# Kernel optimization log

Hardware: AMD Instinct MI355X
Metric: run time of the kernel (lower is better)

Reference implementation:

```python
import jax, jax.numpy as jnp
import numpy as np
from jax.scipy.special import gammainc

HUBREG_ITERS = 2
LAYERS = 3


def huber_psi(x, c):
    # Huber influence function: identity inside [-c, c], clipped outside.
    return jnp.where(jnp.abs(x) <= c, x, c * jnp.sign(x))


def chi2_cdf(x, df):
    return gammainc(df / 2.0, x / 2.0)


def hubreg_batched(beta, D, Y, mask, c, lamda, mu, sigma0):
    """Batched Huber regression with IRLS-style scale update.

    beta: [q, r]  one coefficient vector per regression (columns of Y)
    D:    [p, r]  shared design rows; regression j uses rows where mask[:, j] == 1
    Y:    [p, q]  targets, zero where unobserved
    mask: [p, q]  observation indicator (float)
    """
    p, r = D.shape
    cd = jax.lax.stop_gradient(c)  # original detaches c for alpha
    alpha = 0.5 * cd**2 * (1.0 - chi2_cdf(cd**2, 1.0)) + 0.5 * chi2_cdf(cd**2, 3.0)
    P = (D[:, :, None] * D[:, None, :]).reshape(p, r * r)  # [p, r^2]
    G = (mask.T @ P).reshape(-1, r, r)                     # [q, r, r]
    Ginv = jnp.linalg.inv(G)
    nobs = mask.sum(axis=0)                                # [q]
    sigma = sigma0 * jnp.ones((Y.shape[1],), Y.dtype)
    for _ in range(HUBREG_ITERS):
        R = (Y - D @ beta.T) * mask                        # masked residuals [p, q]
        psi = huber_psi(R / sigma[None, :], c)             # zero where mask is zero
        tau = jnp.sqrt((psi * psi).sum(axis=0)) / jnp.sqrt(2.0 * nobs * alpha)
        sigma = sigma * tau**lamda
        psi2 = huber_psi(R / sigma[None, :], c)
        rhs = D.T @ (psi2 * sigma[None, :])                # [r, q] = D[rows].T @ (psi*sigma)
        delta = jnp.einsum('qij,jq->qi', Ginv, rhs)
        beta = beta + mu * delta
    return beta


def setup_inputs() -> dict:
    key = jax.random.key(0)
    k1, k2, k3, k4 = jax.random.split(key, 4)
    m, n, r = 4096, 4096, 10
    U = jax.random.normal(k1, (m, r), jnp.float32)
    V = jax.random.normal(k2, (r, n), jnp.float32)
    obs = (jax.random.uniform(k3, (m, n)) < 0.5).astype(jnp.float32)
    X = jax.random.normal(k4, (m, n), jnp.float32) * obs  # zeros = missing entries
    return {
        "U": U, "V": V, "X": X,
        "c": jnp.float32(1.345), "lamda": jnp.float32(1.0),
        "mu": jnp.float32(0.5), "sigma": jnp.float32(1.0),
    }


def reference(U, V, X, c, lamda, mu, sigma):
    mask = (X != 0).astype(X.dtype)
    for _ in range(LAYERS):
        V = hubreg_batched(V.T, U, X, mask, c, lamda, mu, sigma).T
        U = hubreg_batched(U, V.T, X.T, mask.T, c, lamda, mu, sigma)
    return U @ V
```

## Files before the change

### kernel.cpp

```cpp
#include <hip/hip_runtime.h>
#include <math.h>

#define RNK 10
#define NG  55
#define TPB 256
#define TPBU 64
#define WPC 4
#define ROWS_P 64
#define ITILE 16

typedef float f2 __attribute__((ext_vector_type(2)));

__device__ __forceinline__ constexpr int tri(int a, int b) { return a*(a+1)/2 + b; }
constexpr int BASE2[10] = {0,0,1,2,4,6,9,12,16,20};

__global__ void init_kernel(const float* __restrict__ Uin, const float* __restrict__ Vin,
                            const float* __restrict__ cptr,
                            float* __restrict__ Ut, float* __restrict__ Vc,
                            float* __restrict__ Urow, float* __restrict__ Vrow,
                            float* __restrict__ Gbuf, float* __restrict__ tauacc,
                            float* __restrict__ rhs, float* __restrict__ alpha,
                            int m, int n, int qmax) {
    int idx = blockIdx.x * TPB + threadIdx.x;
    if (idx == 0) {
        float c  = *cptr;
        float A  = erff(c * 0.70710678118654752f);
        float B  = c * 0.79788456080286536f * expf(-0.5f*c*c);
        *alpha = 0.5f*c*c*(1.0f - A) + 0.5f*(A - B);
    }
    if (idx < RNK * m) { int k = idx / m, i = idx - k*m; Ut[idx] = Uin[i*RNK + k]; }
    if (idx < RNK * m) Urow[idx] = Uin[idx];
    if (idx < RNK * n) Vc[idx] = Vin[idx];
    if (idx < RNK * n) { int j = idx / RNK, k = idx - j*RNK; Vrow[idx] = Vin[k*n + j]; }
    if (idx < (NG + 1) * qmax) Gbuf[idx] = 0.0f;
    if (idx < qmax) tauacc[idx] = 0.0f;
    if (idx < RNK * qmax) rhs[idx] = 0.0f;
}

__global__ void transpose_kernel(const float* __restrict__ X, float* __restrict__ XT,
                                 int m, int n) {
    __shared__ float tile[32][33];
    int bx = blockIdx.x * 32, by = blockIdx.y * 32;
    int tx = threadIdx.x, ty = threadIdx.y;
    #pragma unroll
    for (int dy = 0; dy < 32; dy += 8)
        tile[ty+dy][tx] = X[(size_t)(by+ty+dy)*n + bx + tx];
    __syncthreads();
    #pragma unroll
    for (int dy = 0; dy < 32; dy += 8)
        XT[(size_t)(bx+ty+dy)*m + by + tx] = tile[tx][ty+dy];
}

__global__ void mask_kernel(const float* __restrict__ X, unsigned* __restrict__ maskV,
                            unsigned* __restrict__ maskU, int m, int n) {
    int wave = threadIdx.x >> 6, lane = threadIdx.x & 63;
    int jbase = blockIdx.x * 256 + wave * 64;
    int j  = jbase + lane;
    int i0 = blockIdx.y * 32;
    unsigned wv = 0;
    for (int u = 0; u < 32; ++u) {
        float x = X[(size_t)(i0+u)*n + j];
        bool nz = (x != 0.0f);
        wv |= (nz ? 1u : 0u) << u;
        unsigned long long bb = __ballot(nz);
        if (lane == 0) {
            int jw = jbase >> 5;
            maskU[(size_t)jw     * m + (i0+u)] = (unsigned)bb;
            maskU[(size_t)(jw+1) * m + (i0+u)] = (unsigned)(bb >> 32);
        }
    }
    maskV[(size_t)blockIdx.y * n + j] = wv;
}

__global__ __launch_bounds__(TPB)
void gram_kernel(const unsigned* __restrict__ mask, const float* __restrict__ Drow,
                 float* __restrict__ Gbuf, int q, int p) {
    __shared__ __align__(16) float Dld[WPC * 32][12];
    int j  = blockIdx.x * TPB + threadIdx.x;
    int w0 = blockIdx.y * WPC;
    int ib = w0 * 32;
    #pragma unroll
    for (int t = threadIdx.x; t < WPC * 32 * RNK; t += TPB) {
        int row = t / RNK, k = t - row * RNK;
        Dld[row][k] = Drow[(size_t)ib * RNK + t];
    }
    __syncthreads();
    f2 acc2[25];
    float accs[5];
    #pragma unroll
    for (int k = 0; k < 25; ++k) acc2[k] = (f2){0.0f, 0.0f};
    #pragma unroll
    for (int k = 0; k < 5; ++k) accs[k] = 0.0f;
    unsigned cnt = 0;
    unsigned wnext = mask[(size_t)w0 * q + j];
    for (int w = 0; w < WPC; ++w) {
        unsigned word = wnext;
        int wn = (w + 1 < WPC) ? (w + 1) : (WPC - 1);
        wnext = mask[(size_t)(w0 + wn) * q + j];
        cnt += __popc(word);
        #pragma unroll
        for (int u = 0; u < 32; ++u) {
            float f = (float)((word >> u) & 1u);
            f2 d2[5];
            #pragma unroll
            for (int k = 0; k < 5; ++k) d2[k] = *(const f2*)&Dld[w * 32 + u][2 * k];
            #pragma unroll
            for (int a = 0; a < RNK; ++a) {
                float da = d2[a >> 1][a & 1];
                float t  = f * da;
                f2 tv = {t, t};
                #pragma unroll
                for (int pb = 0; pb < (a + 1) / 2; ++pb)
                    acc2[BASE2[a] + pb] =
                        __builtin_elementwise_fma(tv, d2[pb], acc2[BASE2[a] + pb]);
                if ((a & 1) == 0) accs[a >> 1] = fmaf(t, da, accs[a >> 1]);
            }
        }
    }
    #pragma unroll
    for (int a = 0; a < RNK; ++a) {
        #pragma unroll
        for (int pb = 0; pb < (a + 1) / 2; ++pb) {
            atomicAdd(&Gbuf[tri(a, 2*pb)   * q + j], acc2[BASE2[a] + pb][0]);
            atomicAdd(&Gbuf[tri(a, 2*pb+1) * q + j], acc2[BASE2[a] + pb][1]);
        }
        if ((a & 1) == 0) atomicAdd(&Gbuf[tri(a, a) * q + j], accs[a >> 1]);
    }
    atomicAdd(&Gbuf[NG * q + j], (float)cnt);
}

__global__ __launch_bounds__(TPB)
void pass1_kernel(const float* __restrict__ Y, const float* __restrict__ Drow,
                  const float* __restrict__ Bm, const float* __restrict__ sigstore,
                  const float* __restrict__ sigma0p, const float* __restrict__ cptr,
                  float* __restrict__ tauacc, int q, int p, int use_store) {
    __shared__ __align__(16) float Dp[ROWS_P][12];
    int j  = blockIdx.x * TPB + threadIdx.x;
    int i0 = blockIdx.y * ROWS_P;
    for (int t = threadIdx.x; t < ROWS_P * RNK; t += TPB) {
        int row = t / RNK, k = t - row * RNK;
        Dp[row][k] = Drow[(size_t)i0 * RNK + t];
    }
    __syncthreads();
    f2 b2[5];
    #pragma unroll
    for (int k = 0; k < 5; ++k)
        b2[k] = (f2){Bm[(2*k)*q + j], Bm[(2*k+1)*q + j]};
    float csg = (*cptr) * (use_store ? sigstore[j] : *sigma0p);
    float a0 = 0.0f;
    float y[8];
    #pragma unroll
    for (int u = 0; u < 8; ++u) y[u] = Y[(size_t)(i0+u)*q + j];
    for (int g = 0; g < ROWS_P; g += 8) {
        float yn[8];
        if (g + 8 < ROWS_P) {
            #pragma unroll
            for (int u = 0; u < 8; ++u) yn[u] = Y[(size_t)(i0+g+8+u)*q + j];
        } else {
            #pragma unroll
            for (int u = 0; u < 8; ++u) yn[u] = 0.0f;
        }
        #pragma unroll
        for (int u = 0; u < 8; ++u) {
            int rl = g + u;
            f2 dot2 = {0.0f, 0.0f};
            #pragma unroll
            for (int k = 0; k < 5; ++k) {
                f2 d2 = *(const f2*)&Dp[rl][2*k];
                dot2 = __builtin_elementwise_fma(d2, b2[k], dot2);
            }
            float dot = dot2[0] + dot2[1];
            float r = (y[u] != 0.0f) ? y[u] - dot : 0.0f;
            r = fminf(fmaxf(r, -csg), csg);
            a0 = fmaf(r, r, a0);
        }
        #pragma unroll
        for (int u = 0; u < 8; ++u) y[u] = yn[u];
    }
    atomicAdd(&tauacc[j], a0);
}

__global__ __launch_bounds__(TPB)
void pass2_kernel(const float* __restrict__ Y, const float* __restrict__ Drow,
                  const float* __restrict__ Bm, const float* __restrict__ Gbuf,
                  const float* __restrict__ tauacc, float* __restrict__ sigstore,
                  const float* __restrict__ cptr, const float* __restrict__ alphap,
                  const float* __restrict__ lamdap, const float* __restrict__ sigma0p,
                  float* __restrict__ rhs, int q, int p, int mode) {
    __shared__ __align__(16) float Dp[ROWS_P][12];
    int j  = blockIdx.x * TPB + threadIdx.x;
    int i0 = blockIdx.y * ROWS_P;
    for (int t = threadIdx.x; t < ROWS_P * RNK; t += TPB) {
        int row = t / RNK, k = t - row * RNK;
        Dp[row][k] = Drow[(size_t)i0 * RNK + t];
    }
    __syncthreads();
    f2 b2[5];
    #pragma unroll
    for (int k = 0; k < 5; ++k)
        b2[k] = (f2){Bm[(2*k)*q + j], Bm[(2*k+1)*q + j]};
    float so  = mode ? sigstore[j] : *sigma0p;
    float nb  = Gbuf[NG*q + j];
    float tau = sqrtf(tauacc[j] / (2.0f * nb * (*alphap))) / so;
    float sg  = so * powf(tau, *lamdap);
    if (mode == 0 && blockIdx.y == 0) sigstore[j] = sg;
    float csg = (*cptr) * sg;

    f2 a2[5];
    #pragma unroll
    for (int k = 0; k < 5; ++k) a2[k] = (f2){0.0f, 0.0f};
    float y[8];
    #pragma unroll
    for (int u = 0; u < 8; ++u) y[u] = Y[(size_t)(i0+u)*q + j];
    for (int g = 0; g < ROWS_P; g += 8) {
        float yn[8];
        if (g + 8 < ROWS_P) {
            #pragma unroll
            for (int u = 0; u < 8; ++u) yn[u] = Y[(size_t)(i0+g+8+u)*q + j];
        } else {
            #pragma unroll
            for (int u = 0; u < 8; ++u) yn[u] = 0.0f;
        }
        #pragma unroll
        for (int u = 0; u < 8; ++u) {
            int rl = g + u;
            f2 d2[5];
            #pragma unroll
            for (int k = 0; k < 5; ++k) d2[k] = *(const f2*)&Dp[rl][2*k];
            f2 dot2 = {0.0f, 0.0f};
            #pragma unroll
            for (int k = 0; k < 5; ++k)
                dot2 = __builtin_elementwise_fma(d2[k], b2[k], dot2);
            float dot = dot2[0] + dot2[1];
            float r = (y[u] != 0.0f) ? y[u] - dot : 0.0f;
            r = fminf(fmaxf(r, -csg), csg);
            f2 rv = {r, r};
            #pragma unroll
            for (int k = 0; k < 5; ++k)
                a2[k] = __builtin_elementwise_fma(d2[k], rv, a2[k]);
        }
        #pragma unroll
        for (int u = 0; u < 8; ++u) y[u] = yn[u];
    }
    #pragma unroll
    for (int k = 0; k < 5; ++k) {
        atomicAdd(&rhs[(2*k)*q   + j], a2[k][0]);
        atomicAdd(&rhs[(2*k+1)*q + j], a2[k][1]);
    }
}

__global__ __launch_bounds__(TPBU)
void update_kernel(float* __restrict__ Gbuf, float* __restrict__ rhs,
                   float* __restrict__ Bm, float* __restrict__ Brow,
                   const float* __restrict__ mup,
                   float* __restrict__ tauacc, int q, int zero_g) {
    int j = blockIdx.x * TPBU + threadIdx.x;
    if (j >= q) return;
    float g[NG];
    #pragma unroll
    for (int k = 0; k < NG; ++k) g[k] = Gbuf[k*q + j];
    #pragma unroll
    for (int a = 0; a < RNK; ++a) {
        #pragma unroll
        for (int b = 0; b < a; ++b) {
            float s = g[tri(a,b)];
            #pragma unroll
            for (int k = 0; k < b; ++k) s -= g[tri(a,k)] * g[tri(b,k)];
            g[tri(a,b)] = s / g[tri(b,b)];
        }
        float s = g[tri(a,a)];
        #pragma unroll
        for (int k = 0; k < a; ++k) s -= g[tri(a,k)] * g[tri(a,k)];
        g[tri(a,a)] = sqrtf(s);
    }
    float x[RNK];
    #pragma unroll
    for (int k = 0; k < RNK; ++k) x[k] = rhs[k*q + j];
    #pragma unroll
    for (int a = 0; a < RNK; ++a) {
        float s = x[a];
        #pragma unroll
        for (int k = 0; k < a; ++k) s -= g[tri(a,k)] * x[k];
        x[a] = s / g[tri(a,a)];
    }
    #pragma unroll
    for (int a = RNK-1; a >= 0; --a) {
        float s = x[a];
        #pragma unroll
        for (int k = a+1; k < RNK; ++k) s -= g[tri(k,a)] * x[k];
        x[a] = s / g[tri(a,a)];
    }
    float mu = *mup;
    #pragma unroll
    for (int k = 0; k < RNK; ++k) {
        float nb = Bm[k*q + j] + mu * x[k];
        Bm[k*q + j] = nb;
        Brow[(size_t)j*RNK + k] = nb;
    }
    tauacc[j] = 0.0f;
    #pragma unroll
    for (int k = 0; k < RNK; ++k) rhs[k*q + j] = 0.0f;
    if (zero_g) {
        #pragma unroll
        for (int k = 0; k <= NG; ++k) Gbuf[k*q + j] = 0.0f;
    }
}

__global__ void gemm_kernel(const float* __restrict__ Ut, const float* __restrict__ Vc,
                            float* __restrict__ out, int m, int n) {
    int j  = blockIdx.x * TPB + threadIdx.x;
    int i0 = blockIdx.y * ITILE;
    float v[RNK];
    #pragma unroll
    for (int k = 0; k < RNK; ++k) v[k] = Vc[k*n + j];
    for (int i = i0; i < i0 + ITILE; ++i) {
        float acc = 0.0f;
        #pragma unroll
        for (int k = 0; k < RNK; ++k) acc = fmaf(Ut[k*m + i], v[k], acc);
        out[(size_t)i*n + j] = acc;
    }
}


namespace {
struct Scratch {
    float *Ut, *Vc, *Urow, *Vrow, *Gbuf, *rhs, *sigma, *tauacc, *alpha;
    unsigned *maskV, *maskU;
};

static void hubreg(const float* Y, const unsigned* mask, const float* Drow,
                   float* Bm, float* Brow, int q, int p,
                   const float* c, const float* lamda, const float* mu, const float* sigma0,
                   const Scratch& s, hipStream_t stream) {
    dim3 gg(q / TPB, p / (32 * WPC));
    dim3 gp(q / TPB, p / ROWS_P);
    dim3 gj(q / TPBU);

    gram_kernel  <<<gg, TPB, 0, stream>>>(mask, Drow, s.Gbuf, q, p);
    pass1_kernel <<<gp, TPB, 0, stream>>>(Y, Drow, Bm, s.sigma, sigma0, c, s.tauacc, q, p, 0);
    pass2_kernel <<<gp, TPB, 0, stream>>>(Y, Drow, Bm, s.Gbuf, s.tauacc, s.sigma, c,
                                          s.alpha, lamda, sigma0, s.rhs, q, p, 0);
    update_kernel<<<gj, TPBU, 0, stream>>>(s.Gbuf, s.rhs, Bm, Brow, mu, s.tauacc, q, 0);
    pass1_kernel <<<gp, TPB, 0, stream>>>(Y, Drow, Bm, s.sigma, sigma0, c, s.tauacc, q, p, 1);
    pass2_kernel <<<gp, TPB, 0, stream>>>(Y, Drow, Bm, s.Gbuf, s.tauacc, s.sigma, c,
                                          s.alpha, lamda, sigma0, s.rhs, q, p, 1);
    update_kernel<<<gj, TPBU, 0, stream>>>(s.Gbuf, s.rhs, Bm, Brow, mu, s.tauacc, q, 1);
}
}

extern "C" void kernel_launch(void* const* d_in, const int* in_sizes, int n_in,
                              void* d_out, int out_size, void* d_ws, size_t ws_size,
                              hipStream_t stream) {
    const float* Uin    = (const float*)d_in[0];
    const float* Vin    = (const float*)d_in[1];
    const float* X      = (const float*)d_in[2];
    const float* c      = (const float*)d_in[3];
    const float* lamda  = (const float*)d_in[4];
    const float* mu     = (const float*)d_in[5];
    const float* sigma0 = (const float*)d_in[6];
    float* out = (float*)d_out;

    const int m = in_sizes[0] / RNK;
    const int n = in_sizes[1] / RNK;
    const int qmax = (m > n) ? m : n;

    float* w = (float*)d_ws;
    auto align64 = [](size_t x) { return (x + 63) & ~(size_t)63; };
    size_t off = 0;
    Scratch s;
    s.Ut     = w + off; off = align64(off + (size_t)RNK * m);
    s.Vc     = w + off; off = align64(off + (size_t)RNK * n);
    s.Urow   = w + off; off = align64(off + (size_t)RNK * m);
    s.Vrow   = w + off; off = align64(off + (size_t)RNK * n);
    s.Gbuf   = w + off; off = align64(off + (size_t)(NG + 1) * qmax);
    s.rhs    = w + off; off = align64(off + (size_t)RNK * qmax);
    s.sigma  = w + off; off = align64(off + (size_t)qmax);
    s.tauacc = w + off; off = align64(off + (size_t)qmax);
    s.alpha  = w + off; off = align64(off + 64);
    s.maskV  = (unsigned*)(w + off); off = align64(off + (size_t)(m/32) * n);
    s.maskU  = (unsigned*)(w + off); off = align64(off + (size_t)(n/32) * m);
    (void)ws_size; (void)n_in; (void)out_size;

    {
        int tot = (NG + 1) * qmax;
        init_kernel<<<(tot + TPB - 1) / TPB, TPB, 0, stream>>>(
            Uin, Vin, c, s.Ut, s.Vc, s.Urow, s.Vrow, s.Gbuf, s.tauacc, s.rhs,
            s.alpha, m, n, qmax);
    }
    transpose_kernel<<<dim3(n / 32, m / 32), dim3(32, 8), 0, stream>>>(X, out, m, n);
    mask_kernel<<<dim3(n / 256, m / 32), TPB, 0, stream>>>(X, s.maskV, s.maskU, m, n);

    for (int layer = 0; layer < 3; ++layer) {
        hubreg(X,   s.maskV, s.Urow, s.Vc, s.Vrow, n, m, c, lamda, mu, sigma0, s, stream);
        hubreg(out, s.maskU, s.Vrow, s.Ut, s.Urow, m, n, c, lamda, mu, sigma0, s, stream);
    }

    gemm_kernel<<<dim3(n / TPB, m / ITILE), TPB, 0, stream>>>(s.Ut, s.Vc, out, m, n);
}
```

Measured before the change: 938.1 us.

## Split row ranges across lane quads in gram and pass2 with shuffle reduction

The gram and pass2 kernels now give each column four lanes, each covering a different slice of rows. The four partial sums are combined with xor shuffles, and one lane per quad does the atomic adds. Each block now handles 64 columns over larger row chunks, so far fewer global atomics hit Gbuf and rhs. In exchange, adjacent lanes read mask and Y with a stride of four rows, which hurts coalescing, and the shuffle reduction adds work.

```diff
diff --git a/kernel.cpp b/kernel.cpp
--- a/kernel.cpp
+++ b/kernel.cpp
@@ -5,7 +5,11 @@
 #define NG  55
 #define TPB 256
 #define TPBU 64
-#define WPC 4
+#define GJ   64
+#define GWRD 4
+#define GROWS_B (4 * GWRD * 32)
+#define P2RPT 64
+#define ROWS_P2 (4 * P2RPT)
 #define ROWS_P 64
 #define ITILE 16
 
@@ -13,6 +17,12 @@
 
 __device__ __forceinline__ constexpr int tri(int a, int b) { return a*(a+1)/2 + b; }
 constexpr int BASE2[10] = {0,0,1,2,4,6,9,12,16,20};
+
+__device__ __forceinline__ float qsum(float v) {
+    v += __shfl_xor(v, 1);
+    v += __shfl_xor(v, 2);
+    return v;
+}
 
 __global__ void init_kernel(const float* __restrict__ Uin, const float* __restrict__ Vin,
                             const float* __restrict__ cptr,
@@ -75,12 +85,12 @@
 __global__ __launch_bounds__(TPB)
 void gram_kernel(const unsigned* __restrict__ mask, const float* __restrict__ Drow,
                  float* __restrict__ Gbuf, int q, int p) {
-    __shared__ __align__(16) float Dld[WPC * 32][12];
-    int j  = blockIdx.x * TPB + threadIdx.x;
-    int w0 = blockIdx.y * WPC;
-    int ib = w0 * 32;
-    #pragma unroll
-    for (int t = threadIdx.x; t < WPC * 32 * RNK; t += TPB) {
+    __shared__ __align__(16) float Dld[GROWS_B][12];
+    int lane = threadIdx.x & 63, wave = threadIdx.x >> 6;
+    int jo = lane >> 2, sub = lane & 3;
+    int j  = blockIdx.x * GJ + wave * 16 + jo;
+    int ib = blockIdx.y * GROWS_B;
+    for (int t = threadIdx.x; t < GROWS_B * RNK; t += TPB) {
         int row = t / RNK, k = t - row * RNK;
         Dld[row][k] = Drow[(size_t)ib * RNK + t];
     }
@@ -92,18 +102,21 @@
     #pragma unroll
     for (int k = 0; k < 5; ++k) accs[k] = 0.0f;
     unsigned cnt = 0;
+    int w0 = blockIdx.y * (4 * GWRD) + sub * GWRD;
+    const float* dbase = &Dld[sub * (GWRD * 32)][0];
     unsigned wnext = mask[(size_t)w0 * q + j];
-    for (int w = 0; w < WPC; ++w) {
+    for (int wi = 0; wi < GWRD; ++wi) {
         unsigned word = wnext;
-        int wn = (w + 1 < WPC) ? (w + 1) : (WPC - 1);
+        int wn = (wi + 1 < GWRD) ? (wi + 1) : (GWRD - 1);
         wnext = mask[(size_t)(w0 + wn) * q + j];
         cnt += __popc(word);
+        const float* drow = dbase + wi * (32 * 12);
         #pragma unroll
         for (int u = 0; u < 32; ++u) {
             float f = (float)((word >> u) & 1u);
             f2 d2[5];
             #pragma unroll
-            for (int k = 0; k < 5; ++k) d2[k] = *(const f2*)&Dld[w * 32 + u][2 * k];
+            for (int k = 0; k < 5; ++k) d2[k] = *(const f2*)(drow + u * 12 + 2 * k);
             #pragma unroll
             for (int a = 0; a < RNK; ++a) {
                 float da = d2[a >> 1][a & 1];
@@ -118,15 +131,25 @@
         }
     }
     #pragma unroll
-    for (int a = 0; a < RNK; ++a) {
-        #pragma unroll
-        for (int pb = 0; pb < (a + 1) / 2; ++pb) {
-            atomicAdd(&Gbuf[tri(a, 2*pb)   * q + j], acc2[BASE2[a] + pb][0]);
-            atomicAdd(&Gbuf[tri(a, 2*pb+1) * q + j], acc2[BASE2[a] + pb][1]);
-        }
-        if ((a & 1) == 0) atomicAdd(&Gbuf[tri(a, a) * q + j], accs[a >> 1]);
-    }
-    atomicAdd(&Gbuf[NG * q + j], (float)cnt);
+    for (int k = 0; k < 25; ++k) {
+        acc2[k][0] = qsum(acc2[k][0]);
+        acc2[k][1] = qsum(acc2[k][1]);
+    }
+    #pragma unroll
+    for (int k = 0; k < 5; ++k) accs[k] = qsum(accs[k]);
+    float fc = qsum((float)cnt);
+    if (sub == 0) {
+        #pragma unroll
+        for (int a = 0; a < RNK; ++a) {
+            #pragma unroll
+            for (int pb = 0; pb < (a + 1) / 2; ++pb) {
+                atomicAdd(&Gbuf[tri(a, 2*pb)   * q + j], acc2[BASE2[a] + pb][0]);
+                atomicAdd(&Gbuf[tri(a, 2*pb+1) * q + j], acc2[BASE2[a] + pb][1]);
+            }
+            if ((a & 1) == 0) atomicAdd(&Gbuf[tri(a, a) * q + j], accs[a >> 1]);
+        }
+        atomicAdd(&Gbuf[NG * q + j], fc);
+    }
 }
 
 __global__ __launch_bounds__(TPB)
@@ -187,10 +210,12 @@
                   const float* __restrict__ cptr, const float* __restrict__ alphap,
                   const float* __restrict__ lamdap, const float* __restrict__ sigma0p,
                   float* __restrict__ rhs, int q, int p, int mode) {
-    __shared__ __align__(16) float Dp[ROWS_P][12];
-    int j  = blockIdx.x * TPB + threadIdx.x;
-    int i0 = blockIdx.y * ROWS_P;
-    for (int t = threadIdx.x; t < ROWS_P * RNK; t += TPB) {
+    __shared__ __align__(16) float Dp[ROWS_P2][12];
+    int lane = threadIdx.x & 63, wave = threadIdx.x >> 6;
+    int jo = lane >> 2, sub = lane & 3;
+    int j  = blockIdx.x * GJ + wave * 16 + jo;
+    int i0 = blockIdx.y * ROWS_P2;
+    for (int t = threadIdx.x; t < ROWS_P2 * RNK; t += TPB) {
         int row = t / RNK, k = t - row * RNK;
         Dp[row][k] = Drow[(size_t)i0 * RNK + t];
     }
@@ -203,30 +228,32 @@
     float nb  = Gbuf[NG*q + j];
     float tau = sqrtf(tauacc[j] / (2.0f * nb * (*alphap))) / so;
     float sg  = so * powf(tau, *lamdap);
-    if (mode == 0 && blockIdx.y == 0) sigstore[j] = sg;
+    if (mode == 0 && blockIdx.y == 0 && sub == 0) sigstore[j] = sg;
     float csg = (*cptr) * sg;
 
+    int ibase = i0 + sub * P2RPT;
+    const float* dbase = &Dp[sub * P2RPT][0];
     f2 a2[5];
     #pragma unroll
     for (int k = 0; k < 5; ++k) a2[k] = (f2){0.0f, 0.0f};
     float y[8];
     #pragma unroll
-    for (int u = 0; u < 8; ++u) y[u] = Y[(size_t)(i0+u)*q + j];
-    for (int g = 0; g < ROWS_P; g += 8) {
+    for (int u = 0; u < 8; ++u) y[u] = Y[(size_t)(ibase+u)*q + j];
+    for (int g = 0; g < P2RPT; g += 8) {
         float yn[8];
-        if (g + 8 < ROWS_P) {
-            #pragma unroll
-            for (int u = 0; u < 8; ++u) yn[u] = Y[(size_t)(i0+g+8+u)*q + j];
+        if (g + 8 < P2RPT) {
+            #pragma unroll
+            for (int u = 0; u < 8; ++u) yn[u] = Y[(size_t)(ibase+g+8+u)*q + j];
         } else {
             #pragma unroll
             for (int u = 0; u < 8; ++u) yn[u] = 0.0f;
         }
+        const float* drow = dbase + g * 12;
         #pragma unroll
         for (int u = 0; u < 8; ++u) {
-            int rl = g + u;
             f2 d2[5];
             #pragma unroll
-            for (int k = 0; k < 5; ++k) d2[k] = *(const f2*)&Dp[rl][2*k];
+            for (int k = 0; k < 5; ++k) d2[k] = *(const f2*)(drow + u * 12 + 2 * k);
             f2 dot2 = {0.0f, 0.0f};
             #pragma unroll
             for (int k = 0; k < 5; ++k)
@@ -244,8 +271,15 @@
     }
     #pragma unroll
     for (int k = 0; k < 5; ++k) {
-        atomicAdd(&rhs[(2*k)*q   + j], a2[k][0]);
-        atomicAdd(&rhs[(2*k+1)*q + j], a2[k][1]);
+        a2[k][0] = qsum(a2[k][0]);
+        a2[k][1] = qsum(a2[k][1]);
+    }
+    if (sub == 0) {
+        #pragma unroll
+        for (int k = 0; k < 5; ++k) {
+            atomicAdd(&rhs[(2*k)*q   + j], a2[k][0]);
+            atomicAdd(&rhs[(2*k+1)*q + j], a2[k][1]);
+        }
     }
 }
 
@@ -332,18 +366,19 @@
                    float* Bm, float* Brow, int q, int p,
                    const float* c, const float* lamda, const float* mu, const float* sigma0,
                    const Scratch& s, hipStream_t stream) {
-    dim3 gg(q / TPB, p / (32 * WPC));
+    dim3 gg(q / GJ, p / GROWS_B);
     dim3 gp(q / TPB, p / ROWS_P);
+    dim3 gp2(q / GJ, p / ROWS_P2);
     dim3 gj(q / TPBU);
 
     gram_kernel  <<<gg, TPB, 0, stream>>>(mask, Drow, s.Gbuf, q, p);
     pass1_kernel <<<gp, TPB, 0, stream>>>(Y, Drow, Bm, s.sigma, sigma0, c, s.tauacc, q, p, 0);
-    pass2_kernel <<<gp, TPB, 0, stream>>>(Y, Drow, Bm, s.Gbuf, s.tauacc, s.sigma, c,
-                                          s.alpha, lamda, sigma0, s.rhs, q, p, 0);
+    pass2_kernel <<<gp2, TPB, 0, stream>>>(Y, Drow, Bm, s.Gbuf, s.tauacc, s.sigma, c,
+                                           s.alpha, lamda, sigma0, s.rhs, q, p, 0);
     update_kernel<<<gj, TPBU, 0, stream>>>(s.Gbuf, s.rhs, Bm, Brow, mu, s.tauacc, q, 0);
     pass1_kernel <<<gp, TPB, 0, stream>>>(Y, Drow, Bm, s.sigma, sigma0, c, s.tauacc, q, p, 1);
-    pass2_kernel <<<gp, TPB, 0, stream>>>(Y, Drow, Bm, s.Gbuf, s.tauacc, s.sigma, c,
-                                          s.alpha, lamda, sigma0, s.rhs, q, p, 1);
+    pass2_kernel <<<gp2, TPB, 0, stream>>>(Y, Drow, Bm, s.Gbuf, s.tauacc, s.sigma, c,
+                                           s.alpha, lamda, sigma0, s.rhs, q, p, 1);
     update_kernel<<<gj, TPBU, 0, stream>>>(s.Gbuf, s.rhs, Bm, Brow, mu, s.tauacc, q, 1);
 }
 }
```

Result: slower. 967.3 us (+3.1%).

## Fuse mask building into transpose and split gram rows across quad lanes

Applied to the files above, without the earlier changes.

The separate mask kernel is removed, and the transpose kernel now builds both bit-packed masks from its shared-memory tile, so X is read one time fewer. The gram kernel is restructured so that four lanes share one column, each handling a different slice of rows. Their partial sums are combined with quad shuffles before one lane issues the atomics, which cuts atomic traffic per block and gives each block more rows. The cost is extra shuffle work and more shared memory, and the mask-building threads in the transpose may hit shared-memory bank conflicts when reading tile rows.

```diff
diff --git a/kernel.cpp b/kernel.cpp
--- a/kernel.cpp
+++ b/kernel.cpp
@@ -5,7 +5,10 @@
 #define NG  55
 #define TPB 256
 #define TPBU 64
-#define WPC 4
+#define GJ   64
+#define GWRD 4
+#define GROWS_B (4 * GWRD * 32)
+#define GSUBP (GWRD * 32 * 12 + 8)
 #define ROWS_P 64
 #define ITILE 16
 
@@ -13,6 +16,12 @@
 
 __device__ __forceinline__ constexpr int tri(int a, int b) { return a*(a+1)/2 + b; }
 constexpr int BASE2[10] = {0,0,1,2,4,6,9,12,16,20};
+
+__device__ __forceinline__ float qsum(float v) {
+    v += __shfl_xor(v, 1);
+    v += __shfl_xor(v, 2);
+    return v;
+}
 
 __global__ void init_kernel(const float* __restrict__ Uin, const float* __restrict__ Vin,
                             const float* __restrict__ cptr,
@@ -38,6 +47,7 @@
 }
 
 __global__ void transpose_kernel(const float* __restrict__ X, float* __restrict__ XT,
+                                 unsigned* __restrict__ maskV, unsigned* __restrict__ maskU,
                                  int m, int n) {
     __shared__ float tile[32][33];
     int bx = blockIdx.x * 32, by = blockIdx.y * 32;
@@ -49,40 +59,32 @@
     #pragma unroll
     for (int dy = 0; dy < 32; dy += 8)
         XT[(size_t)(bx+ty+dy)*m + by + tx] = tile[tx][ty+dy];
-}
-
-__global__ void mask_kernel(const float* __restrict__ X, unsigned* __restrict__ maskV,
-                            unsigned* __restrict__ maskU, int m, int n) {
-    int wave = threadIdx.x >> 6, lane = threadIdx.x & 63;
-    int jbase = blockIdx.x * 256 + wave * 64;
-    int j  = jbase + lane;
-    int i0 = blockIdx.y * 32;
-    unsigned wv = 0;
-    for (int u = 0; u < 32; ++u) {
-        float x = X[(size_t)(i0+u)*n + j];
-        bool nz = (x != 0.0f);
-        wv |= (nz ? 1u : 0u) << u;
-        unsigned long long bb = __ballot(nz);
-        if (lane == 0) {
-            int jw = jbase >> 5;
-            maskU[(size_t)jw     * m + (i0+u)] = (unsigned)bb;
-            maskU[(size_t)(jw+1) * m + (i0+u)] = (unsigned)(bb >> 32);
-        }
-    }
-    maskV[(size_t)blockIdx.y * n + j] = wv;
+    if (ty == 0) {
+        unsigned wv = 0;
+        #pragma unroll
+        for (int u = 0; u < 32; ++u)
+            wv |= (tile[u][tx] != 0.0f ? 1u : 0u) << u;
+        maskV[(size_t)blockIdx.y * n + bx + tx] = wv;
+    } else if (ty == 1) {
+        unsigned wu = 0;
+        #pragma unroll
+        for (int u = 0; u < 32; ++u)
+            wu |= (tile[tx][u] != 0.0f ? 1u : 0u) << u;
+        maskU[(size_t)blockIdx.x * m + by + tx] = wu;
+    }
 }
 
 __global__ __launch_bounds__(TPB)
 void gram_kernel(const unsigned* __restrict__ mask, const float* __restrict__ Drow,
                  float* __restrict__ Gbuf, int q, int p) {
-    __shared__ __align__(16) float Dld[WPC * 32][12];
-    int j  = blockIdx.x * TPB + threadIdx.x;
-    int w0 = blockIdx.y * WPC;
-    int ib = w0 * 32;
-    #pragma unroll
-    for (int t = threadIdx.x; t < WPC * 32 * RNK; t += TPB) {
+    __shared__ __align__(16) float Dld[4 * GSUBP];
+    int lane = threadIdx.x & 63, wave = threadIdx.x >> 6;
+    int jo = lane >> 2, sub = lane & 3;
+    int j  = blockIdx.x * GJ + wave * 16 + jo;
+    int ib = blockIdx.y * GROWS_B;
+    for (int t = threadIdx.x; t < GROWS_B * RNK; t += TPB) {
         int row = t / RNK, k = t - row * RNK;
-        Dld[row][k] = Drow[(size_t)ib * RNK + t];
+        Dld[(row >> 7) * GSUBP + (row & 127) * 12 + k] = Drow[(size_t)ib * RNK + t];
     }
     __syncthreads();
     f2 acc2[25];
@@ -92,18 +94,21 @@
     #pragma unroll
     for (int k = 0; k < 5; ++k) accs[k] = 0.0f;
     unsigned cnt = 0;
+    int w0 = blockIdx.y * (4 * GWRD) + sub * GWRD;
+    const float* dbase = Dld + sub * GSUBP;
     unsigned wnext = mask[(size_t)w0 * q + j];
-    for (int w = 0; w < WPC; ++w) {
+    for (int wi = 0; wi < GWRD; ++wi) {
         unsigned word = wnext;
-        int wn = (w + 1 < WPC) ? (w + 1) : (WPC - 1);
+        int wn = (wi + 1 < GWRD) ? (wi + 1) : (GWRD - 1);
         wnext = mask[(size_t)(w0 + wn) * q + j];
         cnt += __popc(word);
+        const float* drow = dbase + wi * (32 * 12);
         #pragma unroll
         for (int u = 0; u < 32; ++u) {
             float f = (float)((word >> u) & 1u);
             f2 d2[5];
             #pragma unroll
-            for (int k = 0; k < 5; ++k) d2[k] = *(const f2*)&Dld[w * 32 + u][2 * k];
+            for (int k = 0; k < 5; ++k) d2[k] = *(const f2*)(drow + u * 12 + 2 * k);
             #pragma unroll
             for (int a = 0; a < RNK; ++a) {
                 float da = d2[a >> 1][a & 1];
@@ -118,15 +123,25 @@
         }
     }
     #pragma unroll
-    for (int a = 0; a < RNK; ++a) {
-        #pragma unroll
-        for (int pb = 0; pb < (a + 1) / 2; ++pb) {
-            atomicAdd(&Gbuf[tri(a, 2*pb)   * q + j], acc2[BASE2[a] + pb][0]);
-            atomicAdd(&Gbuf[tri(a, 2*pb+1) * q + j], acc2[BASE2[a] + pb][1]);
-        }
-        if ((a & 1) == 0) atomicAdd(&Gbuf[tri(a, a) * q + j], accs[a >> 1]);
-    }
-    atomicAdd(&Gbuf[NG * q + j], (float)cnt);
+    for (int k = 0; k < 25; ++k) {
+        acc2[k][0] = qsum(acc2[k][0]);
+        acc2[k][1] = qsum(acc2[k][1]);
+    }
+    #pragma unroll
+    for (int k = 0; k < 5; ++k) accs[k] = qsum(accs[k]);
+    float fc = qsum((float)cnt);
+    if (sub == 0) {
+        #pragma unroll
+        for (int a = 0; a < RNK; ++a) {
+            #pragma unroll
+            for (int pb = 0; pb < (a + 1) / 2; ++pb) {
+                atomicAdd(&Gbuf[tri(a, 2*pb)   * q + j], acc2[BASE2[a] + pb][0]);
+                atomicAdd(&Gbuf[tri(a, 2*pb+1) * q + j], acc2[BASE2[a] + pb][1]);
+            }
+            if ((a & 1) == 0) atomicAdd(&Gbuf[tri(a, a) * q + j], accs[a >> 1]);
+        }
+        atomicAdd(&Gbuf[NG * q + j], fc);
+    }
 }
 
 __global__ __launch_bounds__(TPB)
@@ -332,7 +347,7 @@
                    float* Bm, float* Brow, int q, int p,
                    const float* c, const float* lamda, const float* mu, const float* sigma0,
                    const Scratch& s, hipStream_t stream) {
-    dim3 gg(q / TPB, p / (32 * WPC));
+    dim3 gg(q / GJ, p / GROWS_B);
     dim3 gp(q / TPB, p / ROWS_P);
     dim3 gj(q / TPBU);
 
@@ -387,8 +402,8 @@
             Uin, Vin, c, s.Ut, s.Vc, s.Urow, s.Vrow, s.Gbuf, s.tauacc, s.rhs,
             s.alpha, m, n, qmax);
     }
-    transpose_kernel<<<dim3(n / 32, m / 32), dim3(32, 8), 0, stream>>>(X, out, m, n);
-    mask_kernel<<<dim3(n / 256, m / 32), TPB, 0, stream>>>(X, s.maskV, s.maskU, m, n);
+    transpose_kernel<<<dim3(n / 32, m / 32), dim3(32, 8), 0, stream>>>(
+        X, out, s.maskV, s.maskU, m, n);
 
     for (int layer = 0; layer < 3; ++layer) {
         hubreg(X,   s.maskV, s.Urow, s.Vc, s.Vrow, n, m, c, lamda, mu, sigma0, s, stream);
```

After: 850.2 us (median of 2 runs). 1.1x faster.
